# Kernel tuning notes

Measured on AMD Instinct MI355X. Metric: run time of the kernel, lower is better.

The kernel has to match this reference:

```python
import jax, jax.numpy as jnp
import numpy as np
import math

LMAX = 4
C = 128
COUT = 128
NLM = (LMAX + 1) ** 2  # 25
# per-m -> l index map: [0,1,1,1,2,...]
LIDX = np.repeat(np.arange(LMAX + 1), [2 * l + 1 for l in range(LMAX + 1)])


def _assoc_legendre(lmax, x):
    # P[l, m, :] associated Legendre (with Condon-Shortley phase) at points x
    P = np.zeros((lmax + 1, lmax + 1, len(x)))
    P[0, 0] = 1.0
    s = np.sqrt(np.clip(1.0 - x * x, 0.0, None))
    for m in range(1, lmax + 1):
        P[m, m] = -(2 * m - 1) * s * P[m - 1, m - 1]
    for m in range(lmax):
        P[m + 1, m] = (2 * m + 1) * x * P[m, m]
    for m in range(lmax + 1):
        for l in range(m + 2, lmax + 1):
            P[l, m] = ((2 * l - 1) * x * P[l - 1, m] - (l + m - 1) * P[l - 2, m]) / (l - m)
    return P


def _s2_grid(lmax):
    # ToS2Grid / FromS2Grid basis: real orthonormal spherical harmonics on a
    # Gauss-Legendre (beta) x uniform (alpha) grid, with exact quadrature so
    # from_grid(to_grid(x)) == x for degrees <= lmax.
    res_beta = 4 * (lmax + 1) if lmax % 2 == 1 else 4 * lmax
    res_alpha = res_beta - 1
    xb, wb = np.polynomial.legendre.leggauss(res_beta)  # x = cos(beta)
    alpha = 2.0 * np.pi * np.arange(res_alpha) / res_alpha
    P = _assoc_legendre(lmax, xb)
    Y = np.zeros((NLM, res_beta, res_alpha))
    i = 0
    for l in range(lmax + 1):
        for m in range(-l, l + 1):
            am = abs(m)
            K = math.sqrt((2 * l + 1) / (4 * math.pi) * math.factorial(l - am) / math.factorial(l + am))
            if m == 0:
                Yb, Ya = K * P[l, 0], np.ones_like(alpha)
            elif m > 0:
                Yb, Ya = math.sqrt(2) * K * P[l, am], np.cos(am * alpha)
            else:
                Yb, Ya = math.sqrt(2) * K * P[l, am], np.sin(am * alpha)
            Y[i] = Yb[:, None] * Ya[None, :]
            i += 1
    wquad = wb * (2.0 * np.pi / res_alpha)
    return Y.astype(np.float32), wquad.astype(np.float32)


_Y_NP, _W_NP = _s2_grid(LMAX)


def setup_inputs() -> dict:
    key = jax.random.key(0)
    k1, k2, k3, k4, k5 = jax.random.split(key, 5)
    B = 16384
    return {
        "feature": jax.random.normal(k1, (B, C * NLM), dtype=jnp.float32),
        "sh": jax.random.normal(k2, (B, NLM), dtype=jnp.float32),
        "w1": jax.random.normal(k3, (C, LMAX + 1), dtype=jnp.float32),
        "w2": jax.random.normal(k4, (LMAX + 1,), dtype=jnp.float32),
        "wc": jax.random.normal(k5, (LMAX + 1, C, COUT), dtype=jnp.float32),
    }


def reference(feature, sh, w1, w2, wc):
    Y = jnp.asarray(_Y_NP)          # [25, 16, 15]
    wq = jnp.asarray(_W_NP)         # [16]
    B = feature.shape[0]
    # preprocess: flat irreps layout [B, C*(2l+1) per l] -> [B, C, 25]
    blocks, off = [], 0
    for l in range(LMAX + 1):
        d = 2 * l + 1
        blocks.append(feature[:, off:off + C * d].reshape(B, C, d))
        off += C * d
    f = jnp.concatenate(blocks, axis=-1)  # [B, C, 25]
    # per-degree weights expanded over m
    image = f * w1[:, LIDX][None]                      # [B, C, 25]
    x1 = jnp.einsum('bci,igh->bcgh', image, Y)         # to S2 grid
    kernel = sh * w2[LIDX][None]                       # [B, 25]
    x2 = jnp.einsum('bi,igh->bgh', kernel, Y)
    x3 = x1 * x2[:, None]                              # elementwise grid product
    feat = jnp.einsum('bcgh,igh,g->bci', x3, Y, wq)    # from S2 grid, [B, C, 25]
    # per-degree channel mixing
    outs = []
    for l in range(LMAX + 1):
        fl = feat[:, :, l * l:(l + 1) * (l + 1)]       # [B, C, 2l+1]
        outs.append(jnp.einsum('bci,ca->bai', fl, wc[l]).reshape(B, -1))
    out = jnp.concatenate(outs, axis=-1)               # [B, COUT*25]
    return out.astype(sh.dtype)
```

## Files before the change

kernel.cpp:

```cpp
#include <hip/hip_runtime.h>
#include <hip/hip_bf16.h>
#include <math.h>


#define NB_TOTAL 16384
#define PLANE ((size_t)NB_TOTAL * 128)

typedef __attribute__((ext_vector_type(8))) short bf16x8;
typedef __attribute__((ext_vector_type(4))) float f32x4;
typedef unsigned short u16;

__constant__ int LTAB[25] = {0, 1,1,1, 2,2,2,2,2, 3,3,3,3,3,3,3, 4,4,4,4,4,4,4,4,4};
__constant__ double FACT[9] = {1.0,1.0,2.0,6.0,24.0,120.0,720.0,5040.0,40320.0};

#define PI_D 3.14159265358979323846

__device__ inline u16 f2bf(float x) {
    __hip_bfloat16 h = __float2bfloat16(x);
    return *reinterpret_cast<u16*>(&h);
}

__global__ void k_nodes(double* __restrict__ XG, double* __restrict__ WG) {
    int g = threadIdx.x;
    if (g >= 16) return;
    double x = cos(PI_D * (g + 0.75) / 16.5);
    for (int it = 0; it < 40; ++it) {
        double p0 = 1.0, p1 = x;
        for (int k = 2; k <= 16; ++k) {
            double pk = ((2.0 * k - 1.0) * x * p1 - (k - 1.0) * p0) / k;
            p0 = p1; p1 = pk;
        }
        double dp = 16.0 * (x * p1 - p0) / (x * x - 1.0);
        x -= p1 / dp;
    }
    double p0 = 1.0, p1 = x;
    for (int k = 2; k <= 16; ++k) {
        double pk = ((2.0 * k - 1.0) * x * p1 - (k - 1.0) * p0) / k;
        p0 = p1; p1 = pk;
    }
    double dp = 16.0 * (x * p1 - p0) / (x * x - 1.0);
    XG[g] = x;
    WG[g] = 2.0 / ((1.0 - x * x) * dp * dp) * (2.0 * PI_D / 15.0);
}

__global__ void k_ylm(const double* __restrict__ XG, float* __restrict__ Y) {
    int i = blockIdx.x;
    int t = threadIdx.x;
    if (t >= 240) return;
    int g = t / 15, h = t % 15;
    int l = LTAB[i];
    int m = i - l * l - l;
    int am = m < 0 ? -m : m;
    double x = XG[g];
    double s = sqrt(fmax(0.0, 1.0 - x * x));
    double P[5][5];
    P[0][0] = 1.0;
    for (int mm = 1; mm <= 4; ++mm) P[mm][mm] = -(2.0 * mm - 1.0) * s * P[mm - 1][mm - 1];
    for (int mm = 0; mm < 4; ++mm)  P[mm + 1][mm] = (2.0 * mm + 1.0) * x * P[mm][mm];
    for (int mm = 0; mm <= 4; ++mm)
        for (int ll = mm + 2; ll <= 4; ++ll)
            P[ll][mm] = ((2.0 * ll - 1.0) * x * P[ll - 1][mm] - (ll + mm - 1.0) * P[ll - 2][mm]) / (ll - mm);
    double K = sqrt((2.0 * l + 1.0) / (4.0 * PI_D) * FACT[l - am] / FACT[l + am]);
    double alpha = 2.0 * PI_D * h / 15.0;
    double v;
    if (m == 0)      v = K * P[l][0];
    else if (m > 0)  v = sqrt(2.0) * K * P[l][am] * cos(am * alpha);
    else             v = sqrt(2.0) * K * P[l][am] * sin(am * alpha);
    Y[i * 240 + g * 15 + h] = (float)v;
}

__global__ void k_gaunt(const float* __restrict__ Y, const double* __restrict__ WG,
                        float* __restrict__ G) {
    int t = blockIdx.x * 256 + threadIdx.x;
    if (t >= 15625) return;
    int i  = t / 625;
    int r  = t % 625;
    int i1 = r / 25;
    int i2 = r % 25;
    const float* y0 = Y + i  * 240;
    const float* y1 = Y + i1 * 240;
    const float* y2 = Y + i2 * 240;
    double acc = 0.0;
    for (int g = 0; g < 16; ++g) {
        double shs = 0.0;
        for (int h = 0; h < 15; ++h) {
            int o = g * 15 + h;
            shs += (double)y0[o] * (double)y1[o] * (double)y2[o];
        }
        acc += WG[g] * shs;
    }
    G[t] = (float)acc;
}

__global__ void k_wcT(const float* __restrict__ wc, u16* __restrict__ wcT) {
    int idx = blockIdx.x * 256 + threadIdx.x;
    if (idx >= 81920) return;
    int l = idx >> 14;
    int r = idx & 16383;
    int c = r >> 7;
    int a = r & 127;
    wcT[(l << 14) + (a << 7) + c] = f2bf(wc[idx]);
}

__global__ __launch_bounds__(256) void k_M(const float* __restrict__ sh,
                                           const float* __restrict__ w2,
                                           const float* __restrict__ G,
                                           float* __restrict__ M) {
    __shared__ float Gs[15625];
    __shared__ float kerns[8 * 25];
    int tid = threadIdx.x;
    int b0 = blockIdx.x * 8;
    for (int t = tid; t < 15625; t += 256) Gs[t] = G[t];
    if (tid < 200) {
        int nb = tid / 25, ii = tid % 25;
        kerns[tid] = sh[(size_t)(b0 + nb) * 25 + ii] * w2[LTAB[ii]];
    }
    __syncthreads();
    for (int e = tid; e < 8 * 625; e += 256) {
        int nb = e / 625;
        int r  = e % 625;
        const float* gr = &Gs[r * 25];
        const float* kr = &kerns[nb * 25];
        float acc = 0.0f;
#pragma unroll
        for (int i2 = 0; i2 < 25; ++i2) acc = fmaf(gr[i2], kr[i2], acc);
        M[(size_t)(b0 + nb) * 625 + r] = acc;
    }
}

__global__ __launch_bounds__(256) void k_feat(const float* __restrict__ feature,
                                              const float* __restrict__ w1,
                                              const float* __restrict__ M,
                                              u16* __restrict__ feat) {
    __shared__ float Ms[4][704];
    int tid = threadIdx.x;
    int wave = tid >> 6, lane = tid & 63;
    int b0 = blockIdx.x << 2;
    for (int t = tid; t < 2500; t += 256) {
        int wb = t / 625, r = t - wb * 625;
        int i = r / 25, i1 = r - i * 25;
        Ms[wb][i * 28 + i1] = M[(size_t)(b0 + wb) * 625 + r];
    }
    __syncthreads();

    int b = b0 + wave;
    int c0 = lane, c1 = lane + 64;
    const float* frow = feature + (size_t)b * 3200;
    float img0[25], img1[25];
    {
        float wa = w1[c0 * 5 + 0], wb_ = w1[c1 * 5 + 0];
        img0[0] = frow[c0] * wa;  img1[0] = frow[c1] * wb_;
        wa = w1[c0 * 5 + 1]; wb_ = w1[c1 * 5 + 1];
#pragma unroll
        for (int j = 0; j < 3; ++j) { img0[1+j] = frow[128 + c0*3 + j] * wa;
                                      img1[1+j] = frow[128 + c1*3 + j] * wb_; }
        wa = w1[c0 * 5 + 2]; wb_ = w1[c1 * 5 + 2];
#pragma unroll
        for (int j = 0; j < 5; ++j) { img0[4+j] = frow[512 + c0*5 + j] * wa;
                                      img1[4+j] = frow[512 + c1*5 + j] * wb_; }
        wa = w1[c0 * 5 + 3]; wb_ = w1[c1 * 5 + 3];
#pragma unroll
        for (int j = 0; j < 7; ++j) { img0[9+j] = frow[1152 + c0*7 + j] * wa;
                                      img1[9+j] = frow[1152 + c1*7 + j] * wb_; }
        wa = w1[c0 * 5 + 4]; wb_ = w1[c1 * 5 + 4];
#pragma unroll
        for (int j = 0; j < 9; ++j) { img0[16+j] = frow[2048 + c0*9 + j] * wa;
                                      img1[16+j] = frow[2048 + c1*9 + j] * wb_; }
    }
    u16* fo = feat + (size_t)b * 128;
#pragma unroll
    for (int i = 0; i < 25; ++i) {
        const float* mr = &Ms[wave][i * 28];
        float a0 = 0.0f, a1 = 0.0f;
#pragma unroll
        for (int q = 0; q < 6; ++q) {
            float4 m4 = *(const float4*)&mr[q * 4];
            a0 = fmaf(img0[q*4+0], m4.x, a0);  a1 = fmaf(img1[q*4+0], m4.x, a1);
            a0 = fmaf(img0[q*4+1], m4.y, a0);  a1 = fmaf(img1[q*4+1], m4.y, a1);
            a0 = fmaf(img0[q*4+2], m4.z, a0);  a1 = fmaf(img1[q*4+2], m4.z, a1);
            a0 = fmaf(img0[q*4+3], m4.w, a0);  a1 = fmaf(img1[q*4+3], m4.w, a1);
        }
        float ml = mr[24];
        a0 = fmaf(img0[24], ml, a0);  a1 = fmaf(img1[24], ml, a1);
        fo[(size_t)i * PLANE + c0] = f2bf(a0);
        fo[(size_t)i * PLANE + c1] = f2bf(a1);
    }
}

template<int L>
__global__ __launch_bounds__(256) void k_out_t(const u16* __restrict__ feat,
                                               const u16* __restrict__ wcT,
                                               float* __restrict__ out) {
    constexpr int D = 2 * L + 1;
    int btile = blockIdx.x << 4;
    int tid = threadIdx.x;
    int wave = tid >> 6, lane = tid & 63;
    int col = lane & 15, quad = lane >> 4;

    const u16* wl = wcT + (L << 14);
    bf16x8 Wf[2][4];
#pragma unroll
    for (int t = 0; t < 2; ++t) {
        int a = ((wave * 2 + t) << 4) + col;
#pragma unroll
        for (int ks = 0; ks < 4; ++ks)
            Wf[t][ks] = *(const bf16x8*)&wl[a * 128 + ks * 32 + (quad << 3)];
    }

    const u16* fbase = feat + (size_t)(L * L) * PLANE
                            + (size_t)(btile + col) * 128 + (quad << 3);
    f32x4 acc[2][D];
#pragma unroll
    for (int t = 0; t < 2; ++t)
#pragma unroll
        for (int j = 0; j < D; ++j) acc[t][j] = (f32x4){0.f, 0.f, 0.f, 0.f};

#pragma unroll
    for (int j = 0; j < D; ++j) {
        const u16* fj = fbase + (size_t)j * PLANE;
#pragma unroll
        for (int ks = 0; ks < 4; ++ks) {
            bf16x8 Af = *(const bf16x8*)&fj[ks * 32];
#pragma unroll
            for (int t = 0; t < 2; ++t)
                acc[t][j] = __builtin_amdgcn_mfma_f32_16x16x32_bf16(Af, Wf[t][ks], acc[t][j], 0, 0, 0);
        }
    }

#pragma unroll
    for (int t = 0; t < 2; ++t) {
        int a = ((wave * 2 + t) << 4) + col;
#pragma unroll
        for (int rg = 0; rg < 4; ++rg) {
            int b = btile + (quad << 2) + rg;
            float* p = out + (size_t)b * 3200 + 128 * L * L + a * D;
#pragma unroll
            for (int j = 0; j < D; ++j) p[j] = acc[t][j][rg];
        }
    }
}

extern "C" void kernel_launch(void* const* d_in, const int* in_sizes, int n_in,
                              void* d_out, int out_size, void* d_ws, size_t ws_size,
                              hipStream_t stream) {
    const float* feature = (const float*)d_in[0];
    const float* sh      = (const float*)d_in[1];
    const float* w1      = (const float*)d_in[2];
    const float* w2      = (const float*)d_in[3];
    const float* wc      = (const float*)d_in[4];
    float* out = (float*)d_out;

    char* w = (char*)d_ws;
    double* XG  = (double*)(w + 0);
    double* WG  = (double*)(w + 128);
    float*  Yf  = (float*)(w + 256);
    float*  Gf  = (float*)(w + 24320);
    u16*    WcT = (u16*)(w + 86912);
    float*  Mf  = (float*)(w + 250880);
    u16*    Ff  = (u16*)(w + 41210880ULL);

    hipLaunchKernelGGL(k_nodes, dim3(1),    dim3(64),  0, stream, XG, WG);
    hipLaunchKernelGGL(k_ylm,   dim3(25),   dim3(256), 0, stream, XG, Yf);
    hipLaunchKernelGGL(k_gaunt, dim3(62),   dim3(256), 0, stream, Yf, WG, Gf);
    hipLaunchKernelGGL(k_wcT,   dim3(320),  dim3(256), 0, stream, wc, WcT);
    hipLaunchKernelGGL(k_M,     dim3(2048), dim3(256), 0, stream, sh, w2, Gf, Mf);
    hipLaunchKernelGGL(k_feat,  dim3(4096), dim3(256), 0, stream, feature, w1, Mf, Ff);
    hipLaunchKernelGGL(k_out_t<0>, dim3(1024), dim3(256), 0, stream, Ff, WcT, out);
    hipLaunchKernelGGL(k_out_t<1>, dim3(1024), dim3(256), 0, stream, Ff, WcT, out);
    hipLaunchKernelGGL(k_out_t<2>, dim3(1024), dim3(256), 0, stream, Ff, WcT, out);
    hipLaunchKernelGGL(k_out_t<3>, dim3(1024), dim3(256), 0, stream, Ff, WcT, out);
    hipLaunchKernelGGL(k_out_t<4>, dim3(1024), dim3(256), 0, stream, Ff, WcT, out);
}
```

Before: 562.1 us.

## Fuse Gaunt contraction, feature projection and channel mixing into one kernel

```diff
diff --git a/kernel.cpp b/kernel.cpp
--- a/kernel.cpp
+++ b/kernel.cpp
@@ -2,9 +2,6 @@
 #include <hip/hip_bf16.h>
 #include <math.h>
 
-
-#define NB_TOTAL 16384
-#define PLANE ((size_t)NB_TOTAL * 128)
 
 typedef __attribute__((ext_vector_type(8))) short bf16x8;
 typedef __attribute__((ext_vector_type(4))) float f32x4;
@@ -102,74 +99,30 @@
     wcT[(l << 14) + (a << 7) + c] = f2bf(wc[idx]);
 }
 
-__global__ __launch_bounds__(256) void k_M(const float* __restrict__ sh,
-                                           const float* __restrict__ w2,
-                                           const float* __restrict__ G,
-                                           float* __restrict__ M) {
-    __shared__ float Gs[15625];
-    __shared__ float kerns[8 * 25];
-    int tid = threadIdx.x;
-    int b0 = blockIdx.x * 8;
-    for (int t = tid; t < 15625; t += 256) Gs[t] = G[t];
-    if (tid < 200) {
-        int nb = tid / 25, ii = tid % 25;
-        kerns[tid] = sh[(size_t)(b0 + nb) * 25 + ii] * w2[LTAB[ii]];
-    }
-    __syncthreads();
-    for (int e = tid; e < 8 * 625; e += 256) {
-        int nb = e / 625;
-        int r  = e % 625;
-        const float* gr = &Gs[r * 25];
-        const float* kr = &kerns[nb * 25];
-        float acc = 0.0f;
-#pragma unroll
-        for (int i2 = 0; i2 < 25; ++i2) acc = fmaf(gr[i2], kr[i2], acc);
-        M[(size_t)(b0 + nb) * 625 + r] = acc;
-    }
-}
-
-__global__ __launch_bounds__(256) void k_feat(const float* __restrict__ feature,
-                                              const float* __restrict__ w1,
-                                              const float* __restrict__ M,
-                                              u16* __restrict__ feat) {
-    __shared__ float Ms[4][704];
-    int tid = threadIdx.x;
-    int wave = tid >> 6, lane = tid & 63;
-    int b0 = blockIdx.x << 2;
-    for (int t = tid; t < 2500; t += 256) {
-        int wb = t / 625, r = t - wb * 625;
-        int i = r / 25, i1 = r - i * 25;
-        Ms[wb][i * 28 + i1] = M[(size_t)(b0 + wb) * 625 + r];
-    }
-    __syncthreads();
-
-    int b = b0 + wave;
-    int c0 = lane, c1 = lane + 64;
-    const float* frow = feature + (size_t)b * 3200;
-    float img0[25], img1[25];
-    {
-        float wa = w1[c0 * 5 + 0], wb_ = w1[c1 * 5 + 0];
-        img0[0] = frow[c0] * wa;  img1[0] = frow[c1] * wb_;
-        wa = w1[c0 * 5 + 1]; wb_ = w1[c1 * 5 + 1];
-#pragma unroll
-        for (int j = 0; j < 3; ++j) { img0[1+j] = frow[128 + c0*3 + j] * wa;
-                                      img1[1+j] = frow[128 + c1*3 + j] * wb_; }
-        wa = w1[c0 * 5 + 2]; wb_ = w1[c1 * 5 + 2];
-#pragma unroll
-        for (int j = 0; j < 5; ++j) { img0[4+j] = frow[512 + c0*5 + j] * wa;
-                                      img1[4+j] = frow[512 + c1*5 + j] * wb_; }
-        wa = w1[c0 * 5 + 3]; wb_ = w1[c1 * 5 + 3];
-#pragma unroll
-        for (int j = 0; j < 7; ++j) { img0[9+j] = frow[1152 + c0*7 + j] * wa;
-                                      img1[9+j] = frow[1152 + c1*7 + j] * wb_; }
-        wa = w1[c0 * 5 + 4]; wb_ = w1[c1 * 5 + 4];
-#pragma unroll
-        for (int j = 0; j < 9; ++j) { img0[16+j] = frow[2048 + c0*9 + j] * wa;
-                                      img1[16+j] = frow[2048 + c1*9 + j] * wb_; }
-    }
-    u16* fo = feat + (size_t)b * 128;
-#pragma unroll
-    for (int i = 0; i < 25; ++i) {
+template<int L>
+__device__ __forceinline__ void do_l(int wave, int lane, int btile,
+                                     const float (&img0)[25], const float (&img1)[25],
+                                     const float (*Ms)[704],
+                                     u16 (*featLDS)[4][144],
+                                     const u16* __restrict__ wcT,
+                                     float* __restrict__ out)
+{
+    constexpr int D = 2 * L + 1;
+    int col = lane & 15, quad = lane >> 4;
+
+    const u16* wl = wcT + (L << 14);
+    bf16x8 Wf[2][4];
+#pragma unroll
+    for (int t = 0; t < 2; ++t) {
+        int a = ((wave * 2 + t) << 4) + col;
+#pragma unroll
+        for (int ks = 0; ks < 4; ++ks)
+            Wf[t][ks] = *(const bf16x8*)&wl[a * 128 + ks * 32 + (quad << 3)];
+    }
+
+#pragma unroll
+    for (int j = 0; j < D; ++j) {
+        int i = L * L + j;
         const float* mr = &Ms[wave][i * 28];
         float a0 = 0.0f, a1 = 0.0f;
 #pragma unroll
@@ -182,62 +135,106 @@
         }
         float ml = mr[24];
         a0 = fmaf(img0[24], ml, a0);  a1 = fmaf(img1[24], ml, a1);
-        fo[(size_t)i * PLANE + c0] = f2bf(a0);
-        fo[(size_t)i * PLANE + c1] = f2bf(a1);
-    }
-}
-
-template<int L>
-__global__ __launch_bounds__(256) void k_out_t(const u16* __restrict__ feat,
-                                               const u16* __restrict__ wcT,
-                                               float* __restrict__ out) {
-    constexpr int D = 2 * L + 1;
-    int btile = blockIdx.x << 4;
+        featLDS[j][wave][lane]      = f2bf(a0);
+        featLDS[j][wave][lane + 64] = f2bf(a1);
+    }
+    __syncthreads();
+
+#pragma unroll
+    for (int jb = 0; jb < D; jb += 4) {
+        int nj = D - jb; if (nj > 4) nj = 4;
+        const u16* arow = &featLDS[jb + (col >> 2)][col & 3][quad << 3];
+        f32x4 acc0 = (f32x4){0.f, 0.f, 0.f, 0.f};
+        f32x4 acc1 = (f32x4){0.f, 0.f, 0.f, 0.f};
+#pragma unroll
+        for (int ks = 0; ks < 4; ++ks) {
+            bf16x8 Af = *(const bf16x8*)&arow[ks * 32];
+            acc0 = __builtin_amdgcn_mfma_f32_16x16x32_bf16(Af, Wf[0][ks], acc0, 0, 0, 0);
+            acc1 = __builtin_amdgcn_mfma_f32_16x16x32_bf16(Af, Wf[1][ks], acc1, 0, 0, 0);
+        }
+        if (quad < nj) {
+            int j = jb + quad;
+#pragma unroll
+            for (int t = 0; t < 2; ++t) {
+                int a = ((wave * 2 + t) << 4) + col;
+                const f32x4& ac = t ? acc1 : acc0;
+#pragma unroll
+                for (int rg = 0; rg < 4; ++rg)
+                    out[(size_t)(btile + rg) * 3200 + 128 * L * L + a * D + j] = ac[rg];
+            }
+        }
+    }
+    __syncthreads();
+}
+
+__global__ __launch_bounds__(256, 2) void k_fused(
+        const float* __restrict__ feature, const float* __restrict__ sh,
+        const float* __restrict__ w1, const float* __restrict__ w2,
+        const float* __restrict__ G, const u16* __restrict__ wcT,
+        float* __restrict__ out)
+{
+    __shared__ alignas(16) u16   featLDS[12][4][144];
+    __shared__ alignas(16) float Ms[4][704];
+    __shared__ float kerns[4][25];
+
     int tid = threadIdx.x;
     int wave = tid >> 6, lane = tid & 63;
-    int col = lane & 15, quad = lane >> 4;
-
-    const u16* wl = wcT + (L << 14);
-    bf16x8 Wf[2][4];
-#pragma unroll
-    for (int t = 0; t < 2; ++t) {
-        int a = ((wave * 2 + t) << 4) + col;
-#pragma unroll
-        for (int ks = 0; ks < 4; ++ks)
-            Wf[t][ks] = *(const bf16x8*)&wl[a * 128 + ks * 32 + (quad << 3)];
-    }
-
-    const u16* fbase = feat + (size_t)(L * L) * PLANE
-                            + (size_t)(btile + col) * 128 + (quad << 3);
-    f32x4 acc[2][D];
-#pragma unroll
-    for (int t = 0; t < 2; ++t)
-#pragma unroll
-        for (int j = 0; j < D; ++j) acc[t][j] = (f32x4){0.f, 0.f, 0.f, 0.f};
-
-#pragma unroll
-    for (int j = 0; j < D; ++j) {
-        const u16* fj = fbase + (size_t)j * PLANE;
-#pragma unroll
-        for (int ks = 0; ks < 4; ++ks) {
-            bf16x8 Af = *(const bf16x8*)&fj[ks * 32];
-#pragma unroll
-            for (int t = 0; t < 2; ++t)
-                acc[t][j] = __builtin_amdgcn_mfma_f32_16x16x32_bf16(Af, Wf[t][ks], acc[t][j], 0, 0, 0);
-        }
-    }
-
-#pragma unroll
-    for (int t = 0; t < 2; ++t) {
-        int a = ((wave * 2 + t) << 4) + col;
-#pragma unroll
-        for (int rg = 0; rg < 4; ++rg) {
-            int b = btile + (quad << 2) + rg;
-            float* p = out + (size_t)b * 3200 + 128 * L * L + a * D;
-#pragma unroll
-            for (int j = 0; j < D; ++j) p[j] = acc[t][j][rg];
-        }
-    }
+    int btile = blockIdx.x << 2;
+
+    if (tid < 100) {
+        int nb = tid / 25, i2 = tid - nb * 25;
+        kerns[nb][i2] = sh[(size_t)(btile + nb) * 25 + i2] * w2[LTAB[i2]];
+    }
+
+    int b = btile + wave;
+    const float* frow = feature + (size_t)b * 3200;
+    int c0 = lane, c1 = lane + 64;
+    float img0[25], img1[25];
+    {
+        float wa = w1[c0 * 5 + 0], wb_ = w1[c1 * 5 + 0];
+        img0[0] = frow[c0] * wa;  img1[0] = frow[c1] * wb_;
+        wa = w1[c0 * 5 + 1]; wb_ = w1[c1 * 5 + 1];
+#pragma unroll
+        for (int j = 0; j < 3; ++j) { img0[1+j] = frow[128 + c0*3 + j] * wa;
+                                      img1[1+j] = frow[128 + c1*3 + j] * wb_; }
+        wa = w1[c0 * 5 + 2]; wb_ = w1[c1 * 5 + 2];
+#pragma unroll
+        for (int j = 0; j < 5; ++j) { img0[4+j] = frow[512 + c0*5 + j] * wa;
+                                      img1[4+j] = frow[512 + c1*5 + j] * wb_; }
+        wa = w1[c0 * 5 + 3]; wb_ = w1[c1 * 5 + 3];
+#pragma unroll
+        for (int j = 0; j < 7; ++j) { img0[9+j] = frow[1152 + c0*7 + j] * wa;
+                                      img1[9+j] = frow[1152 + c1*7 + j] * wb_; }
+        wa = w1[c0 * 5 + 4]; wb_ = w1[c1 * 5 + 4];
+#pragma unroll
+        for (int j = 0; j < 9; ++j) { img0[16+j] = frow[2048 + c0*9 + j] * wa;
+                                      img1[16+j] = frow[2048 + c1*9 + j] * wb_; }
+    }
+
+    __syncthreads();
+
+    for (int r = tid; r < 625; r += 256) {
+        const float* gr = G + r * 25;
+        float a0 = 0.f, a1 = 0.f, a2 = 0.f, a3 = 0.f;
+#pragma unroll
+        for (int i2 = 0; i2 < 25; ++i2) {
+            float gv = gr[i2];
+            a0 = fmaf(gv, kerns[0][i2], a0);
+            a1 = fmaf(gv, kerns[1][i2], a1);
+            a2 = fmaf(gv, kerns[2][i2], a2);
+            a3 = fmaf(gv, kerns[3][i2], a3);
+        }
+        int i = r / 25, i1 = r - i * 25;
+        int o = i * 28 + i1;
+        Ms[0][o] = a0; Ms[1][o] = a1; Ms[2][o] = a2; Ms[3][o] = a3;
+    }
+    __syncthreads();
+
+    do_l<0>(wave, lane, btile, img0, img1, Ms, featLDS, wcT, out);
+    do_l<1>(wave, lane, btile, img0, img1, Ms, featLDS, wcT, out);
+    do_l<2>(wave, lane, btile, img0, img1, Ms, featLDS, wcT, out);
+    do_l<3>(wave, lane, btile, img0, img1, Ms, featLDS, wcT, out);
+    do_l<4>(wave, lane, btile, img0, img1, Ms, featLDS, wcT, out);
 }
 
 extern "C" void kernel_launch(void* const* d_in, const int* in_sizes, int n_in,
@@ -255,19 +252,12 @@
     double* WG  = (double*)(w + 128);
     float*  Yf  = (float*)(w + 256);
     float*  Gf  = (float*)(w + 24320);
-    u16*    WcT = (u16*)(w + 86912);
-    float*  Mf  = (float*)(w + 250880);
-    u16*    Ff  = (u16*)(w + 41210880ULL);
+    u16*    WcT = (u16*)(w + 87040);
 
     hipLaunchKernelGGL(k_nodes, dim3(1),    dim3(64),  0, stream, XG, WG);
     hipLaunchKernelGGL(k_ylm,   dim3(25),   dim3(256), 0, stream, XG, Yf);
     hipLaunchKernelGGL(k_gaunt, dim3(62),   dim3(256), 0, stream, Yf, WG, Gf);
     hipLaunchKernelGGL(k_wcT,   dim3(320),  dim3(256), 0, stream, wc, WcT);
-    hipLaunchKernelGGL(k_M,     dim3(2048), dim3(256), 0, stream, sh, w2, Gf, Mf);
-    hipLaunchKernelGGL(k_feat,  dim3(4096), dim3(256), 0, stream, feature, w1, Mf, Ff);
-    hipLaunchKernelGGL(k_out_t<0>, dim3(1024), dim3(256), 0, stream, Ff, WcT, out);
-    hipLaunchKernelGGL(k_out_t<1>, dim3(1024), dim3(256), 0, stream, Ff, WcT, out);
-    hipLaunchKernelGGL(k_out_t<2>, dim3(1024), dim3(256), 0, stream, Ff, WcT, out);
-    hipLaunchKernelGGL(k_out_t<3>, dim3(1024), dim3(256), 0, stream, Ff, WcT, out);
-    hipLaunchKernelGGL(k_out_t<4>, dim3(1024), dim3(256), 0, stream, Ff, WcT, out);
-}
+    hipLaunchKernelGGL(k_fused, dim3(4096), dim3(256), 0, stream,
+                       feature, sh, w1, w2, Gf, WcT, out);
+}
```

Measured after the change: 456.7 us. 18.7% less time.
